# Kernel tuning notes

Hardware: AMD Instinct MI355X
Metric: run time of the kernel (lower is better)

## Reference

```python
import jax, jax.numpy as jnp
import numpy as np
import math

PHI = (1 + math.sqrt(5)) / 2
PI = math.pi
B, N, T, D, H = 2, 16, 512, 512, 8
DH = D // H
HALF = DH // 2
FF = int(D * PHI)  # 828
DC = D
PR_EPS = 1e-8
LN_EPS = 1e-5


def _ln(x, g, b):
    # x: (B,N,T,D); g,b: (N,D)
    mu = x.mean(axis=-1, keepdims=True)
    var = ((x - mu) ** 2).mean(axis=-1, keepdims=True)
    return (x - mu) * jax.lax.rsqrt(var + LN_EPS) * g[None, :, None, :] + b[None, :, None, :]


def _phase_resonance(a, b):
    # a, b: (B, N, D) in fp32; adjacent feature pairs = (re, im)
    pairs = a.shape[-1] // 2
    def to_phase(x):
        x2 = x.reshape(*x.shape[:-1], pairs, 2)
        return jnp.arctan2(x2[..., 1] + PR_EPS, x2[..., 0] + PR_EPS)
    ta, tb = to_phase(a), to_phase(b)
    delta = ta[..., :, None, :] - tb[..., None, :, :]  # (B, N, N, pairs)
    return jnp.cos(delta).mean(axis=-1)                # (B, N, N) in [-1, 1]


def setup_inputs():
    key = jax.random.key(0)
    ks = iter(jax.random.split(key, 24))
    w = lambda shape: jax.random.normal(next(ks), shape, jnp.float32) * 0.02
    return {
        'x': jax.random.normal(next(ks), (B, N, T, D), jnp.float32),
        'gate_w': w((N, D)),
        'gate_b': jnp.full((N,), 2.0, jnp.float32),  # torch init: bias=2.0
        'ln1_g': jnp.ones((N, D), jnp.float32),
        'ln1_b': jnp.zeros((N, D), jnp.float32),
        'wq': w((N, D, D)), 'wk': w((N, D, D)), 'wv': w((N, D, D)), 'wo': w((N, D, D)),
        'phase_angles': jnp.tile(jnp.linspace(0.0, PI, H, dtype=jnp.float32), (N, 1)),
        'ln2_g': jnp.ones((N, D), jnp.float32),
        'ln2_b': jnp.zeros((N, D), jnp.float32),
        'up_w': w((N, D, FF)), 'up_b': jnp.zeros((N, FF), jnp.float32),
        'down_w': w((N, FF, D)), 'down_b': jnp.zeros((N, D), jnp.float32),
        'commit_w': w((N, D)), 'commit_b': jnp.zeros((N,), jnp.float32),
        'center_w': w((N, D, DC)), 'center_b': jnp.zeros((N, DC), jnp.float32),
        'field_in_w': w((D, D)),
        'field_out_w': w((D, D)),
        'conductance': jnp.float32(1.0),
    }


def reference(x, gate_w, gate_b, ln1_g, ln1_b, wq, wk, wv, wo, phase_angles,
              ln2_g, ln2_b, up_w, up_b, down_w, down_b, commit_w, commit_b,
              center_w, center_b, field_in_w, field_out_w, conductance):
    # ---- BinaryAperture (straight-through binary gate) ----
    logits = jnp.einsum('bntd,nd->bnt', x, gate_w) + gate_b[None, :, None]
    prob = jax.nn.sigmoid(logits)  # temperature = 1.0
    hard = (prob > 0.5).astype(x.dtype)
    gate = (hard + prob - jax.lax.stop_gradient(prob))[..., None]  # (B,N,T,1)

    # ---- Field: phase-rotated, gated attention (scores forced to fp32) ----
    h = _ln(x, ln1_g, ln1_b)
    def proj(wm):
        z = jnp.einsum('bntd,nde->bnte', h, wm)
        return z.reshape(B, N, T, H, DH).transpose(0, 1, 3, 2, 4)  # (B,N,H,T,DH)
    Q, K, V = proj(wq), proj(wk), proj(wv)
    cos_a = jnp.cos(phase_angles)[None, :, :, None, None]  # (1,N,H,1,1)
    sin_a = jnp.sin(phase_angles)[None, :, :, None, None]
    def rot(Z):
        re, im = Z[..., :HALF], Z[..., HALF:2 * HALF]
        return jnp.concatenate([re * cos_a - im * sin_a, re * sin_a + im * cos_a], axis=-1)
    Q, K = rot(Q), rot(K)
    ge = gate[:, :, None]  # (B,N,1,T,1) broadcast over heads
    Q = Q * ge
    K = K * ge
    scores = jnp.einsum('bnhtd,bnhsd->bnhts', Q.astype(jnp.float32), K.astype(jnp.float32)) / math.sqrt(DH)
    attn = jax.nn.softmax(scores, axis=-1).astype(V.dtype)
    field = jnp.einsum('bnhts,bnhsd->bnhtd', attn, V)
    field = field.transpose(0, 1, 3, 2, 4).reshape(B, N, T, D)
    field = jnp.einsum('bntd,nde->bnte', field, wo) * gate
    x = x + field

    # ---- Boundary: golden-ratio FFN gated by commit * gate ----
    h2 = _ln(x, ln2_g, ln2_b)
    up = jax.nn.gelu(jnp.einsum('bntd,ndf->bntf', h2, up_w) + up_b[None, :, None], approximate=False)
    ff = jnp.einsum('bntf,nfd->bntd', up, down_w) + down_b[None, :, None]
    center_pool = x.mean(axis=2)  # (B,N,D) (pooled pre-FFN, as in torch)
    commit = jax.nn.sigmoid(jnp.einsum('bnd,nd->bn', center_pool, commit_w) + commit_b[None])  # (B,N)
    x = x + commit[..., None, None] * gate * ff
    center = jnp.tanh(jnp.einsum('bnd,nde->bne', center_pool, center_w) + center_b[None])  # (B,N,DC)

    # ---- SharedField: phase-resonance coupling across the N nodes ----
    node_gates = commit[..., None]  # (B,N,1)
    transmitted = center * node_gates
    h_res = jnp.einsum('bnd,de->bne', center, field_in_w).astype(jnp.float32)
    r_acc = _phase_resonance(h_res, h_res)  # (B,N,N); r_acc None -> r_acc_new = r_instant
    h_tx = jnp.einsum('bnd,de->bne', transmitted, field_in_w)
    recv = conductance * jnp.einsum('bmn,bnd->bmd', r_acc.astype(x.dtype), h_tx)
    field_signal = jnp.einsum('bnd,de->bne', recv, field_out_w)  # (B,N,D)

    # each node's boundary receives the field signal
    return x + field_signal[:, :, None, :]
```

## Files before the change

### kernel.cpp

```cpp
#include <hip/hip_runtime.h>

typedef unsigned short u16;
typedef __attribute__((ext_vector_type(8))) short short8;
typedef __attribute__((ext_vector_type(4))) float f32x4;

#define B_ 2
#define N_ 16
#define T_ 512
#define D_ 512
#define H_ 8
#define DH_ 64
#define HALF_ 32
#define FF_ 828
#define FFP_ 832
#define DC_ 512
#define LN_EPS 1e-5f
#define PR_EPS 1e-8f
#define NEG_INF (-3.0e38f)

__device__ __forceinline__ float b2f(u16 u) { return __uint_as_float(((unsigned)u) << 16); }
__device__ __forceinline__ u16 f2b(float f) {
  unsigned x = __float_as_uint(f);
  return (u16)((x + 0x7fffu + ((x >> 16) & 1u)) >> 16);
}
__device__ __forceinline__ float gelu_exact(float z) {
  return 0.5f * z * (1.f + erff(z * 0.70710678118654752f));
}

typedef __attribute__((address_space(1))) const unsigned GASu;
typedef __attribute__((address_space(3))) unsigned LASu;
__device__ __forceinline__ void gload_lds16(const void* g, void* l) {
  __builtin_amdgcn_global_load_lds((GASu*)g, (LASu*)l, 16, 0, 0);
}

__global__ __launch_bounds__(256) void ln_gate_kernel(
    const float* __restrict__ xsrc,
    const float* __restrict__ gate_w, const float* __restrict__ gate_b,
    const float* __restrict__ lng, const float* __restrict__ lnb,
    float* __restrict__ gate_out, u16* __restrict__ h_out, int do_gate) {
  __shared__ float red[256];
  int bnt = blockIdx.x;
  int n = (bnt / T_) % N_;
  int tid = threadIdx.x;
  const float* xr = xsrc + (size_t)bnt * D_;
  float x0 = xr[tid], x1 = xr[tid + 256];
  red[tid] = x0 + x1; __syncthreads();
  for (int s = 128; s > 0; s >>= 1) { if (tid < s) red[tid] += red[tid + s]; __syncthreads(); }
  float mu = red[0] * (1.f / D_); __syncthreads();
  float d0 = x0 - mu, d1 = x1 - mu;
  red[tid] = d0 * d0 + d1 * d1; __syncthreads();
  for (int s = 128; s > 0; s >>= 1) { if (tid < s) red[tid] += red[tid + s]; __syncthreads(); }
  float rstd = rsqrtf(red[0] * (1.f / D_) + LN_EPS); __syncthreads();
  if (do_gate) {
    red[tid] = x0 * gate_w[n * D_ + tid] + x1 * gate_w[n * D_ + tid + 256];
    __syncthreads();
    for (int s = 128; s > 0; s >>= 1) { if (tid < s) red[tid] += red[tid + s]; __syncthreads(); }
    if (tid == 0) gate_out[bnt] = (red[0] + gate_b[n] > 0.f) ? 1.f : 0.f;
  }
  size_t o = (size_t)bnt * D_;
  h_out[o + tid]       = f2b(d0 * rstd * lng[n * D_ + tid]       + lnb[n * D_ + tid]);
  h_out[o + tid + 256] = f2b(d1 * rstd * lng[n * D_ + tid + 256] + lnb[n * D_ + tid + 256]);
}

__global__ __launch_bounds__(256) void wconv_kernel(
    const float* __restrict__ W, u16* __restrict__ Wt, int Kd, int E, int Kpad) {
  __shared__ u16 tile[32][33];
  int e0 = blockIdx.x * 32, k0 = blockIdx.y * 32, n = blockIdx.z;
  const float* Wb = W + (size_t)n * Kd * E;
  u16* Wtb = Wt + (size_t)n * E * Kpad;
  int r = threadIdx.x >> 3, c4 = (threadIdx.x & 7) * 4;
  int kk = k0 + r;
  if (kk < Kd) {
    if (e0 + c4 + 3 < E) {
      float4 w4 = *(const float4*)(Wb + (size_t)kk * E + e0 + c4);
      tile[r][c4 + 0] = f2b(w4.x); tile[r][c4 + 1] = f2b(w4.y);
      tile[r][c4 + 2] = f2b(w4.z); tile[r][c4 + 3] = f2b(w4.w);
    } else {
      #pragma unroll
      for (int j = 0; j < 4; ++j) {
        int ee = e0 + c4 + j;
        tile[r][c4 + j] = (ee < E) ? f2b(Wb[(size_t)kk * E + ee]) : (u16)0;
      }
    }
  } else {
    #pragma unroll
    for (int j = 0; j < 4; ++j) tile[r][c4 + j] = 0;
  }
  __syncthreads();
  int ee = e0 + r;
  if (ee < E) {
    u16* dst = Wtb + (size_t)ee * Kpad + k0 + c4;
    if (k0 + c4 + 3 < Kpad) {
      ushort4 o;
      o.x = tile[c4 + 0][r]; o.y = tile[c4 + 1][r];
      o.z = tile[c4 + 2][r]; o.w = tile[c4 + 3][r];
      *(ushort4*)dst = o;
    } else {
      #pragma unroll
      for (int j = 0; j < 4; ++j) if (k0 + c4 + j < Kpad) dst[j] = tile[c4 + j][r];
    }
  }
}

#define BM 128
#define BN 128
#define BK 32
__global__ __launch_bounds__(256) void gemm_mfma_kernel(
    const u16* __restrict__ In,
    const float* __restrict__ W0, const float* __restrict__ W1, const float* __restrict__ W2,
    const u16* __restrict__ Wt0, const u16* __restrict__ Wt1, const u16* __restrict__ Wt2,
    u16* __restrict__ O0, u16* __restrict__ O1, u16* __restrict__ O2,
    float* __restrict__ OutF,
    int Kd, int KdW, int E, int Es, int mode,
    const float* __restrict__ bias,
    const float* __restrict__ xres, const float* __restrict__ gate) {
  __shared__ __align__(16) u16 As[BM * BK];
  __shared__ __align__(16) u16 Bs[BN * BK];
  int z = blockIdx.z;
  int bn = z & 31, proj = z >> 5;
  int n = bn & (N_ - 1);
  const float* W = (proj == 0) ? W0 : ((proj == 1) ? W1 : W2);
  const u16* Wt = (proj == 0) ? Wt0 : ((proj == 1) ? Wt1 : Wt2);
  u16* Out = (proj == 0) ? O0 : ((proj == 1) ? O1 : O2);
  int e0 = blockIdx.x * BN, t0 = blockIdx.y * BM;
  int tid = threadIdx.x;
  int lane = tid & 63, wave = tid >> 6;
  int m_off = (wave & 1) * 64, n_off = (wave >> 1) * 64;
  int ml = lane & 15, quad = lane >> 4;
  const u16* Inb = In + (size_t)bn * T_ * Kd;
  const float* Wb = W ? W + (size_t)n * (size_t)KdW * E : nullptr;
  const u16* Wtb = Wt ? Wt + (size_t)n * E * Kd : nullptr;

  int srow = (wave * 2) * 16 + (lane >> 2);
  int sg0 = (lane & 3) ^ ((srow >> 1) & 3);
  int sg1 = (lane & 3) ^ (((srow + 16) >> 1) & 3);
  int swz = (quad ^ ((ml >> 1) & 3)) * 8;

  f32x4 acc[4][4] = {};

  int ksteps = (Kd + BK - 1) / BK;
  for (int ks = 0; ks < ksteps; ++ks) {
    int k0 = ks * BK;
    if (Wtb) {
      int i0 = wave * 2;
      gload_lds16(Inb + (size_t)(t0 + srow) * Kd + k0 + sg0 * 8, &As[i0 * 512]);
      gload_lds16(Inb + (size_t)(t0 + srow + 16) * Kd + k0 + sg1 * 8, &As[(i0 + 1) * 512]);
      gload_lds16(Wtb + (size_t)(e0 + srow) * Kd + k0 + sg0 * 8, &Bs[i0 * 512]);
      gload_lds16(Wtb + (size_t)(e0 + srow + 16) * Kd + k0 + sg1 * 8, &Bs[(i0 + 1) * 512]);
    } else {
      #pragma unroll
      for (int it = 0; it < 2; ++it) {
        int slot = tid * 2 + it;
        int r = slot >> 2;
        int q = slot & 3;
        int kg = k0 + q * 8;
        const u16* src = Inb + (size_t)(t0 + r) * Kd + kg;
        u16* dst = &As[r * BK + (q ^ ((r >> 1) & 3)) * 8];
        if (kg + 8 <= Kd) {
          *(short8*)dst = *(const short8*)src;
        } else {
          #pragma unroll
          for (int xx = 0; xx < 8; ++xx) dst[xx] = (kg + xx < Kd) ? src[xx] : (u16)0;
        }
      }
      {
        int kk = tid & 31;
        int eb = (tid >> 5) * 16;
        int kg = k0 + kk;
        int s = kk >> 3, w = kk & 7;
        #pragma unroll
        for (int it = 0; it < 4; ++it) {
          int e = eb + it * 4;
          int eg = e0 + e;
          float4 w4 = {0.f, 0.f, 0.f, 0.f};
          if (kg < KdW && eg < E) w4 = *(const float4*)(Wb + (size_t)kg * E + eg);
          Bs[(e + 0) * BK + ((s ^ (((e + 0) >> 1) & 3)) * 8) + w] = f2b(w4.x);
          Bs[(e + 1) * BK + ((s ^ (((e + 1) >> 1) & 3)) * 8) + w] = f2b(w4.y);
          Bs[(e + 2) * BK + ((s ^ (((e + 2) >> 1) & 3)) * 8) + w] = f2b(w4.z);
          Bs[(e + 3) * BK + ((s ^ (((e + 3) >> 1) & 3)) * 8) + w] = f2b(w4.w);
        }
      }
    }
    __syncthreads();
    short8 a[4], b[4];
    #pragma unroll
    for (int i = 0; i < 4; ++i)
      a[i] = *(const short8*)&As[(m_off + i * 16 + ml) * BK + swz];
    #pragma unroll
    for (int j = 0; j < 4; ++j)
      b[j] = *(const short8*)&Bs[(n_off + j * 16 + ml) * BK + swz];
    #pragma unroll
    for (int i = 0; i < 4; ++i)
      #pragma unroll
      for (int j = 0; j < 4; ++j)
        acc[i][j] = __builtin_amdgcn_mfma_f32_16x16x32_bf16(a[i], b[j], acc[i][j], 0, 0, 0);
    __syncthreads();
  }

  #pragma unroll
  for (int j = 0; j < 4; ++j) {
    int eg = e0 + n_off + j * 16 + ml;
    if (eg >= Es) continue;
    #pragma unroll
    for (int i = 0; i < 4; ++i) {
      #pragma unroll
      for (int r = 0; r < 4; ++r) {
        int tg = t0 + m_off + i * 16 + quad * 4 + r;
        float v = acc[i][j][r];
        size_t o = (size_t)bn * T_ * Es + (size_t)tg * Es + eg;
        if (mode == 0) {
          Out[o] = f2b(v);
        } else if (mode == 1) {
          float g = gate[(size_t)bn * T_ + tg];
          OutF[o] = xres[o] + v * g;
        } else if (mode == 2) {
          Out[o] = (eg < E) ? f2b(gelu_exact(v + bias[(size_t)n * E + eg])) : (u16)0;
        } else {
          Out[o] = f2b(v + bias[(size_t)n * E + eg]);
        }
      }
    }
  }
}

__global__ __launch_bounds__(256) void rot_gate_kernel(
    u16* __restrict__ q, u16* __restrict__ k,
    const float* __restrict__ phase, const float* __restrict__ gate) {
  long long i = (long long)blockIdx.x * 256 + threadIdx.x;
  int c = (int)(i & 31);
  int h = (int)((i >> 5) & 7);
  int t = (int)((i >> 8) & 511);
  int bn = (int)(i >> 17);
  int n = bn & (N_ - 1);
  float a = phase[n * H_ + h];
  float ca = cosf(a), sa = sinf(a);
  float g = gate[(size_t)bn * T_ + t];
  size_t base = ((size_t)bn * T_ + t) * D_ + h * DH_;
  float qr = b2f(q[base + c]), qi = b2f(q[base + c + HALF_]);
  q[base + c]         = f2b((qr * ca - qi * sa) * g);
  q[base + c + HALF_] = f2b((qr * sa + qi * ca) * g);
  float kr = b2f(k[base + c]), ki = b2f(k[base + c + HALF_]);
  k[base + c]         = f2b((kr * ca - ki * sa) * g);
  k[base + c + HALF_] = f2b((kr * sa + ki * ca) * g);
}

#define ATS 72
__global__ __launch_bounds__(256) void attn_kernel(
    const u16* __restrict__ Q, const u16* __restrict__ K, const u16* __restrict__ V,
    u16* __restrict__ O) {
  __shared__ __align__(16) u16 Qs[64 * ATS];
  __shared__ __align__(16) u16 Ks[64 * ATS];
  __shared__ __align__(16) u16 Vs[64 * ATS];
  __shared__ __align__(16) u16 Ps[64 * ATS];
  int qt = blockIdx.x, h = blockIdx.y, bn = blockIdx.z;
  int tid = threadIdx.x;
  int lane = tid & 63, wave = tid >> 6;
  int ml = lane & 15, quad = lane >> 4;
  int t0 = qt * 64;
  size_t rowbase = (size_t)bn * T_ * D_ + (size_t)h * DH_;

  {
    int r = tid >> 2;
    int c = (tid & 3) * 16;
    const u16* src = Q + rowbase + (size_t)(t0 + r) * D_ + c;
    #pragma unroll
    for (int hf = 0; hf < 2; ++hf) {
      short8 v = *(const short8*)(src + hf * 8);
      #pragma unroll
      for (int e = 0; e < 8; ++e)
        ((u16*)&v)[e] = f2b(b2f(((u16*)&v)[e]) * 0.125f);
      *(short8*)&Qs[r * ATS + c + hf * 8] = v;
    }
  }

  float m_[4], l_[4];
  f32x4 acco[4] = {};
  #pragma unroll
  for (int r = 0; r < 4; ++r) { m_[r] = NEG_INF; l_[r] = 0.f; }

  for (int sc = 0; sc < 8; ++sc) {
    int s0 = sc * 64;
    {
      int r = tid >> 2;
      int c = (tid & 3) * 16;
      const u16* src = K + rowbase + (size_t)(s0 + r) * D_ + c;
      *(short8*)&Ks[r * ATS + c]     = *(const short8*)(src);
      *(short8*)&Ks[r * ATS + c + 8] = *(const short8*)(src + 8);
    }
    {
      int sw = wave * 16;
      const u16* src = V + rowbase + (size_t)(s0 + sw) * D_ + lane;
      short8 v0, v1;
      #pragma unroll
      for (int r = 0; r < 8; ++r) ((u16*)&v0)[r] = src[(size_t)r * D_];
      #pragma unroll
      for (int r = 0; r < 8; ++r) ((u16*)&v1)[r] = src[(size_t)(r + 8) * D_];
      *(short8*)&Vs[lane * ATS + sw]     = v0;
      *(short8*)&Vs[lane * ATS + sw + 8] = v1;
    }
    __syncthreads();

    f32x4 s4[4] = {};
    #pragma unroll
    for (int kst = 0; kst < 2; ++kst) {
      short8 a = *(const short8*)&Qs[(wave * 16 + ml) * ATS + kst * 32 + quad * 8];
      #pragma unroll
      for (int j = 0; j < 4; ++j) {
        short8 b = *(const short8*)&Ks[(j * 16 + ml) * ATS + kst * 32 + quad * 8];
        s4[j] = __builtin_amdgcn_mfma_f32_16x16x32_bf16(a, b, s4[j], 0, 0, 0);
      }
    }

    #pragma unroll
    for (int r = 0; r < 4; ++r) {
      float cm = fmaxf(fmaxf(s4[0][r], s4[1][r]), fmaxf(s4[2][r], s4[3][r]));
      #pragma unroll
      for (int off = 1; off < 16; off <<= 1) cm = fmaxf(cm, __shfl_xor(cm, off));
      float mn = fmaxf(m_[r], cm);
      float al = expf(m_[r] - mn);
      u16 q0 = f2b(expf(s4[0][r] - mn)), q1 = f2b(expf(s4[1][r] - mn));
      u16 q2 = f2b(expf(s4[2][r] - mn)), q3 = f2b(expf(s4[3][r] - mn));
      float rs = b2f(q0) + b2f(q1) + b2f(q2) + b2f(q3);
      #pragma unroll
      for (int off = 1; off < 16; off <<= 1) rs += __shfl_xor(rs, off);
      l_[r] = l_[r] * al + rs;
      m_[r] = mn;
      #pragma unroll
      for (int jd = 0; jd < 4; ++jd) acco[jd][r] *= al;
      int trow = wave * 16 + quad * 4 + r;
      Ps[trow * ATS + 0 * 16 + ml] = q0;
      Ps[trow * ATS + 1 * 16 + ml] = q1;
      Ps[trow * ATS + 2 * 16 + ml] = q2;
      Ps[trow * ATS + 3 * 16 + ml] = q3;
    }

    #pragma unroll
    for (int sst = 0; sst < 2; ++sst) {
      short8 a = *(const short8*)&Ps[(wave * 16 + ml) * ATS + sst * 32 + quad * 8];
      #pragma unroll
      for (int jd = 0; jd < 4; ++jd) {
        short8 b = *(const short8*)&Vs[(jd * 16 + ml) * ATS + sst * 32 + quad * 8];
        acco[jd] = __builtin_amdgcn_mfma_f32_16x16x32_bf16(a, b, acco[jd], 0, 0, 0);
      }
    }
    __syncthreads();
  }

  #pragma unroll
  for (int r = 0; r < 4; ++r) {
    float inv = 1.f / l_[r];
    int trow = t0 + wave * 16 + quad * 4 + r;
    #pragma unroll
    for (int jd = 0; jd < 4; ++jd)
      O[rowbase + (size_t)trow * D_ + jd * 16 + ml] = f2b(acco[jd][r] * inv);
  }
}

__global__ __launch_bounds__(256) void pool_kernel(const float* __restrict__ x2, float* __restrict__ cp) {
  int bid = blockIdx.x;
  int bn = bid >> 1;
  int d = (bid & 1) * 256 + threadIdx.x;
  const float* base = x2 + (size_t)bn * T_ * D_ + d;
  float s = 0.f;
  for (int t = 0; t < T_; ++t) s += base[(size_t)t * D_];
  cp[(size_t)bn * D_ + d] = s * (1.f / T_);
}

__global__ __launch_bounds__(256) void commit_center_kernel(
    const float* __restrict__ cp, const float* __restrict__ commit_w, const float* __restrict__ commit_b,
    const float* __restrict__ center_w, const float* __restrict__ center_b,
    float* __restrict__ commit, float* __restrict__ center) {
  __shared__ float cps[512];
  __shared__ float red[256];
  int bn = blockIdx.x, n = bn % N_, tid = threadIdx.x;
  cps[tid] = cp[(size_t)bn * D_ + tid];
  cps[tid + 256] = cp[(size_t)bn * D_ + tid + 256];
  __syncthreads();
  red[tid] = cps[tid] * commit_w[n * D_ + tid] + cps[tid + 256] * commit_w[n * D_ + tid + 256];
  __syncthreads();
  for (int s = 128; s > 0; s >>= 1) { if (tid < s) red[tid] += red[tid + s]; __syncthreads(); }
  if (tid == 0) commit[bn] = 1.f / (1.f + expf(-(red[0] + commit_b[n])));
  #pragma unroll
  for (int eo = 0; eo < 2; ++eo) {
    int e = eo * 256 + tid;
    float acc = center_b[(size_t)n * DC_ + e];
    for (int d = 0; d < D_; ++d) acc = fmaf(cps[d], center_w[((size_t)n * D_ + d) * DC_ + e], acc);
    center[(size_t)bn * DC_ + e] = tanhf(acc);
  }
}

__global__ __launch_bounds__(256) void matvec_kernel(
    const float* __restrict__ inp, const float* __restrict__ Wm, float* __restrict__ outp) {
  __shared__ float s[512];
  int bn = blockIdx.x, tid = threadIdx.x;
  s[tid] = inp[(size_t)bn * D_ + tid];
  s[tid + 256] = inp[(size_t)bn * D_ + tid + 256];
  __syncthreads();
  #pragma unroll
  for (int eo = 0; eo < 2; ++eo) {
    int e = eo * 256 + tid;
    float acc = 0.f;
    for (int d = 0; d < D_; ++d) acc = fmaf(s[d], Wm[(size_t)d * D_ + e], acc);
    outp[(size_t)bn * D_ + e] = acc;
  }
}

__global__ __launch_bounds__(256) void uv_kernel(
    const float* __restrict__ hres, float* __restrict__ u, float* __restrict__ v) {
  int i = blockIdx.x * 256 + threadIdx.x;
  float xr = hres[2 * i] + PR_EPS;
  float yi = hres[2 * i + 1] + PR_EPS;
  float r = sqrtf(xr * xr + yi * yi);
  u[i] = xr / r; v[i] = yi / r;
}

__global__ __launch_bounds__(256) void racc_kernel(
    const float* __restrict__ u, const float* __restrict__ v, float* __restrict__ ra) {
  int b = blockIdx.x, tid = threadIdx.x;
  int mm = tid >> 4, nn = tid & 15;
  const float* ub = u + (size_t)b * N_ * 256;
  const float* vb = v + (size_t)b * N_ * 256;
  float acc = 0.f;
  for (int p = 0; p < 256; ++p)
    acc += ub[mm * 256 + p] * ub[nn * 256 + p] + vb[mm * 256 + p] * vb[nn * 256 + p];
  ra[(size_t)b * N_ * N_ + mm * N_ + nn] = acc * (1.f / 256.f);
}

__global__ __launch_bounds__(256) void recv_kernel(
    const float* __restrict__ ra, const float* __restrict__ commit,
    const float* __restrict__ hres, const float* __restrict__ cond, float* __restrict__ recv) {
  int bn = blockIdx.x, b = bn / N_, mm = bn % N_, tid = threadIdx.x;
  float c = cond[0];
  #pragma unroll
  for (int eo = 0; eo < 2; ++eo) {
    int d = eo * 256 + tid;
    float acc = 0.f;
    for (int nn = 0; nn < N_; ++nn)
      acc += ra[(size_t)b * N_ * N_ + mm * N_ + nn] * commit[b * N_ + nn] *
             hres[((size_t)b * N_ + nn) * D_ + d];
    recv[(size_t)bn * D_ + d] = c * acc;
  }
}

__global__ __launch_bounds__(256) void final_kernel(
    const float* __restrict__ x2, const float* __restrict__ commit,
    const float* __restrict__ gate, const u16* __restrict__ ff,
    const float* __restrict__ fs, float* __restrict__ out) {
  long long i4 = (long long)blockIdx.x * 256 + threadIdx.x;
  long long base = i4 * 4;
  int d = (int)(base & (D_ - 1));
  int t = (int)((base >> 9) & (T_ - 1));
  int bn = (int)(base >> 18);
  float cg = commit[bn] * gate[(size_t)bn * T_ + t];
  float4 xv = *(const float4*)(x2 + base);
  ushort4 fv = *(const ushort4*)(ff + base);
  float4 sv = *(const float4*)(fs + (size_t)bn * D_ + d);
  float4 r;
  r.x = xv.x + cg * b2f(fv.x) + sv.x;
  r.y = xv.y + cg * b2f(fv.y) + sv.y;
  r.z = xv.z + cg * b2f(fv.z) + sv.z;
  r.w = xv.w + cg * b2f(fv.w) + sv.w;
  *(float4*)(out + base) = r;
}

extern "C" void kernel_launch(void* const* d_in, const int* in_sizes, int n_in,
                              void* d_out, int out_size, void* d_ws, size_t ws_size,
                              hipStream_t stream) {
  (void)in_sizes; (void)n_in; (void)out_size;
  const float* x          = (const float*)d_in[0];
  const float* gate_w     = (const float*)d_in[1];
  const float* gate_b     = (const float*)d_in[2];
  const float* ln1_g      = (const float*)d_in[3];
  const float* ln1_b      = (const float*)d_in[4];
  const float* wq         = (const float*)d_in[5];
  const float* wk         = (const float*)d_in[6];
  const float* wv         = (const float*)d_in[7];
  const float* wo         = (const float*)d_in[8];
  const float* phase      = (const float*)d_in[9];
  const float* ln2_g      = (const float*)d_in[10];
  const float* ln2_b      = (const float*)d_in[11];
  const float* up_w       = (const float*)d_in[12];
  const float* up_b       = (const float*)d_in[13];
  const float* down_w     = (const float*)d_in[14];
  const float* down_b     = (const float*)d_in[15];
  const float* commit_w   = (const float*)d_in[16];
  const float* commit_b   = (const float*)d_in[17];
  const float* center_w   = (const float*)d_in[18];
  const float* center_b   = (const float*)d_in[19];
  const float* field_in_w = (const float*)d_in[20];
  const float* field_out_w= (const float*)d_in[21];
  const float* cond       = (const float*)d_in[22];

  const long long BNTD = 8388608LL;
  u16* w16 = (u16*)d_ws;
  u16* R0 = w16;
  u16* R1 = w16 + BNTD;
  u16* R2 = w16 + 2 * BNTD;
  u16* R3 = w16 + 3 * BNTD;
  float* sm   = (float*)(w16 + 4 * BNTD);
  float* gate   = sm;
  float* cp     = sm + 16384;
  float* center = sm + 2 * 16384;
  float* hres   = sm + 3 * 16384;
  float* uu     = sm + 4 * 16384;
  float* vv     = uu + 8192;
  float* ra     = vv + 8192;
  float* recvb  = ra + 512;
  float* fsig   = recvb + 16384;
  float* commit = fsig + 16384;
  float* x2 = (float*)d_out;

  const size_t WSQ = (size_t)N_ * 512 * 512;
  const size_t WUPu = (size_t)N_ * 828 * 512;
  const size_t WUPd = (size_t)N_ * 512 * 832;
  u16* wtbase = (u16*)(sm + 115232);
  u16* wtq = wtbase;
  u16* wtk = wtq + WSQ;
  u16* wtv = wtk + WSQ;
  u16* wto = wtv + WSQ;
  u16* wtu = wto + WSQ;
  u16* wtd = wtu + WUPu;
  size_t needed = (size_t)((char*)(wtd + WUPd) - (char*)d_ws);
  bool use_wt = ws_size >= needed;

  ln_gate_kernel<<<16384, 256, 0, stream>>>(x, gate_w, gate_b, ln1_g, ln1_b, gate, R0, 1);

  if (use_wt) {
    wconv_kernel<<<dim3(16, 16, 16), 256, 0, stream>>>(wq, wtq, 512, 512, 512);
    wconv_kernel<<<dim3(16, 16, 16), 256, 0, stream>>>(wk, wtk, 512, 512, 512);
    wconv_kernel<<<dim3(16, 16, 16), 256, 0, stream>>>(wv, wtv, 512, 512, 512);
    wconv_kernel<<<dim3(16, 16, 16), 256, 0, stream>>>(wo, wto, 512, 512, 512);
    wconv_kernel<<<dim3(26, 16, 16), 256, 0, stream>>>(up_w, wtu, 512, 828, 512);
    wconv_kernel<<<dim3(16, 26, 16), 256, 0, stream>>>(down_w, wtd, 828, 512, 832);
  }
  const u16* pq = use_wt ? wtq : nullptr;
  const u16* pk = use_wt ? wtk : nullptr;
  const u16* pv = use_wt ? wtv : nullptr;
  const u16* po = use_wt ? wto : nullptr;
  const u16* pu = use_wt ? wtu : nullptr;
  const u16* pd = use_wt ? wtd : nullptr;

  gemm_mfma_kernel<<<dim3(4, 4, 96), 256, 0, stream>>>(
      R0, wq, wk, wv, pq, pk, pv, R1, R2, R3, nullptr,
      512, 512, 512, 512, 0, nullptr, nullptr, nullptr);
  rot_gate_kernel<<<16384, 256, 0, stream>>>(R1, R2, phase, gate);
  attn_kernel<<<dim3(8, 8, 32), 256, 0, stream>>>(R1, R2, R3, R0);
  gemm_mfma_kernel<<<dim3(4, 4, 32), 256, 0, stream>>>(
      R0, wo, nullptr, nullptr, po, nullptr, nullptr, nullptr, nullptr, nullptr, x2,
      512, 512, 512, 512, 1, nullptr, x, gate);
  ln_gate_kernel<<<16384, 256, 0, stream>>>(x2, nullptr, nullptr, ln2_g, ln2_b, nullptr, R1, 0);
  gemm_mfma_kernel<<<dim3(7, 4, 32), 256, 0, stream>>>(
      R1, up_w, nullptr, nullptr, pu, nullptr, nullptr, R2, nullptr, nullptr, nullptr,
      512, 512, 828, 832, 2, up_b, nullptr, nullptr);
  gemm_mfma_kernel<<<dim3(4, 4, 32), 256, 0, stream>>>(
      R2, down_w, nullptr, nullptr, pd, nullptr, nullptr, R0, nullptr, nullptr, nullptr,
      832, 828, 512, 512, 3, down_b, nullptr, nullptr);
  pool_kernel<<<64, 256, 0, stream>>>(x2, cp);
  commit_center_kernel<<<32, 256, 0, stream>>>(cp, commit_w, commit_b, center_w, center_b, commit, center);
  matvec_kernel<<<32, 256, 0, stream>>>(center, field_in_w, hres);
  uv_kernel<<<32, 256, 0, stream>>>(hres, uu, vv);
  racc_kernel<<<2, 256, 0, stream>>>(uu, vv, ra);
  recv_kernel<<<32, 256, 0, stream>>>(ra, commit, hres, cond, recvb);
  matvec_kernel<<<32, 256, 0, stream>>>(recvb, field_out_w, fsig);
  final_kernel<<<8192, 256, 0, stream>>>(x2, commit, gate, R0, fsig, x2);
}
```

Baseline: 812.0 us.

## Use wave-shuffle LayerNorm, pre-transposed V, lazy softmax rescale, split pooling

LayerNorm and gate reductions move from shared-memory tree loops to wave shuffles with fewer barriers. A new transpose kernel writes V as (bh, dh, T) so attention loads it with vector loads instead of strided scalar loads. The query scaling by 0.125 moves into the rotary kernel, and the online softmax rescales only when the running max grows, using fast exp. Mean pooling becomes a two-stage parallel reduction with far more blocks. The costs are an extra V transpose pass and extra workspace, and the fast exp may change numerics slightly.

```diff
diff --git a/kernel.cpp b/kernel.cpp
--- a/kernel.cpp
+++ b/kernel.cpp
@@ -38,25 +38,34 @@
     const float* __restrict__ gate_w, const float* __restrict__ gate_b,
     const float* __restrict__ lng, const float* __restrict__ lnb,
     float* __restrict__ gate_out, u16* __restrict__ h_out, int do_gate) {
-  __shared__ float red[256];
+  __shared__ float redA[4], redB[4], redC[4];
   int bnt = blockIdx.x;
   int n = (bnt / T_) % N_;
   int tid = threadIdx.x;
+  int lane = tid & 63, wave = tid >> 6;
   const float* xr = xsrc + (size_t)bnt * D_;
   float x0 = xr[tid], x1 = xr[tid + 256];
-  red[tid] = x0 + x1; __syncthreads();
-  for (int s = 128; s > 0; s >>= 1) { if (tid < s) red[tid] += red[tid + s]; __syncthreads(); }
-  float mu = red[0] * (1.f / D_); __syncthreads();
+  float s = x0 + x1;
+  #pragma unroll
+  for (int off = 32; off > 0; off >>= 1) s += __shfl_xor(s, off);
+  if (lane == 0) redA[wave] = s;
+  if (do_gate) {
+    float t = x0 * gate_w[n * D_ + tid] + x1 * gate_w[n * D_ + tid + 256];
+    #pragma unroll
+    for (int off = 32; off > 0; off >>= 1) t += __shfl_xor(t, off);
+    if (lane == 0) redC[wave] = t;
+  }
+  __syncthreads();
+  float mu = (redA[0] + redA[1] + redA[2] + redA[3]) * (1.f / D_);
   float d0 = x0 - mu, d1 = x1 - mu;
-  red[tid] = d0 * d0 + d1 * d1; __syncthreads();
-  for (int s = 128; s > 0; s >>= 1) { if (tid < s) red[tid] += red[tid + s]; __syncthreads(); }
-  float rstd = rsqrtf(red[0] * (1.f / D_) + LN_EPS); __syncthreads();
-  if (do_gate) {
-    red[tid] = x0 * gate_w[n * D_ + tid] + x1 * gate_w[n * D_ + tid + 256];
-    __syncthreads();
-    for (int s = 128; s > 0; s >>= 1) { if (tid < s) red[tid] += red[tid + s]; __syncthreads(); }
-    if (tid == 0) gate_out[bnt] = (red[0] + gate_b[n] > 0.f) ? 1.f : 0.f;
-  }
+  float v = d0 * d0 + d1 * d1;
+  #pragma unroll
+  for (int off = 32; off > 0; off >>= 1) v += __shfl_xor(v, off);
+  if (lane == 0) redB[wave] = v;
+  __syncthreads();
+  float rstd = rsqrtf((redB[0] + redB[1] + redB[2] + redB[3]) * (1.f / D_) + LN_EPS);
+  if (do_gate && tid == 0)
+    gate_out[bnt] = (redC[0] + redC[1] + redC[2] + redC[3] + gate_b[n] > 0.f) ? 1.f : 0.f;
   size_t o = (size_t)bnt * D_;
   h_out[o + tid]       = f2b(d0 * rstd * lng[n * D_ + tid]       + lnb[n * D_ + tid]);
   h_out[o + tid + 256] = f2b(d1 * rstd * lng[n * D_ + tid + 256] + lnb[n * D_ + tid + 256]);
@@ -100,6 +109,23 @@
       for (int j = 0; j < 4; ++j) if (k0 + c4 + j < Kpad) dst[j] = tile[c4 + j][r];
     }
   }
+}
+
+__global__ __launch_bounds__(256) void vtrans_kernel(const u16* __restrict__ V, u16* __restrict__ Vt) {
+  __shared__ u16 tile[32][36];
+  int tt0 = blockIdx.x * 32;
+  int dd0 = blockIdx.y * 32;
+  int bh = blockIdx.z;
+  int bn = bh >> 3, h = bh & 7;
+  const u16* src = V + (size_t)bn * T_ * D_ + h * DH_;
+  int r = threadIdx.x >> 3, c4 = (threadIdx.x & 7) * 4;
+  *(ushort4*)&tile[r][c4] = *(const ushort4*)(src + (size_t)(tt0 + r) * D_ + dd0 + c4);
+  __syncthreads();
+  u16* dst = Vt + ((size_t)bh * DH_ + dd0 + r) * T_ + tt0 + c4;
+  ushort4 o;
+  o.x = tile[c4 + 0][r]; o.y = tile[c4 + 1][r];
+  o.z = tile[c4 + 2][r]; o.w = tile[c4 + 3][r];
+  *(ushort4*)dst = o;
 }
 
 #define BM 128
@@ -237,8 +263,10 @@
   float g = gate[(size_t)bn * T_ + t];
   size_t base = ((size_t)bn * T_ + t) * D_ + h * DH_;
   float qr = b2f(q[base + c]), qi = b2f(q[base + c + HALF_]);
-  q[base + c]         = f2b((qr * ca - qi * sa) * g);
-  q[base + c + HALF_] = f2b((qr * sa + qi * ca) * g);
+  u16 a0 = f2b((qr * ca - qi * sa) * g);
+  u16 a1 = f2b((qr * sa + qi * ca) * g);
+  q[base + c]         = f2b(b2f(a0) * 0.125f);
+  q[base + c + HALF_] = f2b(b2f(a1) * 0.125f);
   float kr = b2f(k[base + c]), ki = b2f(k[base + c + HALF_]);
   k[base + c]         = f2b((kr * ca - ki * sa) * g);
   k[base + c + HALF_] = f2b((kr * sa + ki * ca) * g);
@@ -247,7 +275,7 @@
 #define ATS 72
 __global__ __launch_bounds__(256) void attn_kernel(
     const u16* __restrict__ Q, const u16* __restrict__ K, const u16* __restrict__ V,
-    u16* __restrict__ O) {
+    const u16* __restrict__ Vt, u16* __restrict__ O) {
   __shared__ __align__(16) u16 Qs[64 * ATS];
   __shared__ __align__(16) u16 Ks[64 * ATS];
   __shared__ __align__(16) u16 Vs[64 * ATS];
@@ -258,43 +286,41 @@
   int ml = lane & 15, quad = lane >> 4;
   int t0 = qt * 64;
   size_t rowbase = (size_t)bn * T_ * D_ + (size_t)h * DH_;
+  int r = tid >> 2;
+  int c = (tid & 3) * 16;
 
   {
-    int r = tid >> 2;
-    int c = (tid & 3) * 16;
     const u16* src = Q + rowbase + (size_t)(t0 + r) * D_ + c;
-    #pragma unroll
-    for (int hf = 0; hf < 2; ++hf) {
-      short8 v = *(const short8*)(src + hf * 8);
-      #pragma unroll
-      for (int e = 0; e < 8; ++e)
-        ((u16*)&v)[e] = f2b(b2f(((u16*)&v)[e]) * 0.125f);
-      *(short8*)&Qs[r * ATS + c + hf * 8] = v;
-    }
-  }
+    *(short8*)&Qs[r * ATS + c]     = *(const short8*)(src);
+    *(short8*)&Qs[r * ATS + c + 8] = *(const short8*)(src + 8);
+  }
+  const u16* ksrc = K + rowbase + (size_t)r * D_ + c;
+  const u16* vsrc = Vt ? (Vt + ((size_t)(bn * H_ + h) * DH_ + r) * T_ + c) : nullptr;
 
   float m_[4], l_[4];
   f32x4 acco[4] = {};
   #pragma unroll
-  for (int r = 0; r < 4; ++r) { m_[r] = NEG_INF; l_[r] = 0.f; }
+  for (int rr = 0; rr < 4; ++rr) { m_[rr] = NEG_INF; l_[rr] = 0.f; }
 
   for (int sc = 0; sc < 8; ++sc) {
     int s0 = sc * 64;
     {
-      int r = tid >> 2;
-      int c = (tid & 3) * 16;
-      const u16* src = K + rowbase + (size_t)(s0 + r) * D_ + c;
-      *(short8*)&Ks[r * ATS + c]     = *(const short8*)(src);
-      *(short8*)&Ks[r * ATS + c + 8] = *(const short8*)(src + 8);
-    }
-    {
+      const u16* kp = ksrc + (size_t)s0 * D_;
+      *(short8*)&Ks[r * ATS + c]     = *(const short8*)(kp);
+      *(short8*)&Ks[r * ATS + c + 8] = *(const short8*)(kp + 8);
+    }
+    if (Vt) {
+      const u16* vp = vsrc + s0;
+      *(short8*)&Vs[r * ATS + c]     = *(const short8*)(vp);
+      *(short8*)&Vs[r * ATS + c + 8] = *(const short8*)(vp + 8);
+    } else {
       int sw = wave * 16;
       const u16* src = V + rowbase + (size_t)(s0 + sw) * D_ + lane;
       short8 v0, v1;
       #pragma unroll
-      for (int r = 0; r < 8; ++r) ((u16*)&v0)[r] = src[(size_t)r * D_];
-      #pragma unroll
-      for (int r = 0; r < 8; ++r) ((u16*)&v1)[r] = src[(size_t)(r + 8) * D_];
+      for (int rr = 0; rr < 8; ++rr) ((u16*)&v0)[rr] = src[(size_t)rr * D_];
+      #pragma unroll
+      for (int rr = 0; rr < 8; ++rr) ((u16*)&v1)[rr] = src[(size_t)(rr + 8) * D_];
       *(short8*)&Vs[lane * ATS + sw]     = v0;
       *(short8*)&Vs[lane * ATS + sw + 8] = v1;
     }
@@ -312,22 +338,24 @@
     }
 
     #pragma unroll
-    for (int r = 0; r < 4; ++r) {
-      float cm = fmaxf(fmaxf(s4[0][r], s4[1][r]), fmaxf(s4[2][r], s4[3][r]));
+    for (int rr = 0; rr < 4; ++rr) {
+      float cm = fmaxf(fmaxf(s4[0][rr], s4[1][rr]), fmaxf(s4[2][rr], s4[3][rr]));
       #pragma unroll
       for (int off = 1; off < 16; off <<= 1) cm = fmaxf(cm, __shfl_xor(cm, off));
-      float mn = fmaxf(m_[r], cm);
-      float al = expf(m_[r] - mn);
-      u16 q0 = f2b(expf(s4[0][r] - mn)), q1 = f2b(expf(s4[1][r] - mn));
-      u16 q2 = f2b(expf(s4[2][r] - mn)), q3 = f2b(expf(s4[3][r] - mn));
+      if (cm > m_[rr]) {
+        float al = __expf(m_[rr] - cm);
+        l_[rr] *= al;
+        #pragma unroll
+        for (int jd = 0; jd < 4; ++jd) acco[jd][rr] *= al;
+        m_[rr] = cm;
+      }
+      u16 q0 = f2b(__expf(s4[0][rr] - m_[rr])), q1 = f2b(__expf(s4[1][rr] - m_[rr]));
+      u16 q2 = f2b(__expf(s4[2][rr] - m_[rr])), q3 = f2b(__expf(s4[3][rr] - m_[rr]));
       float rs = b2f(q0) + b2f(q1) + b2f(q2) + b2f(q3);
       #pragma unroll
       for (int off = 1; off < 16; off <<= 1) rs += __shfl_xor(rs, off);
-      l_[r] = l_[r] * al + rs;
-      m_[r] = mn;
-      #pragma unroll
-      for (int jd = 0; jd < 4; ++jd) acco[jd][r] *= al;
-      int trow = wave * 16 + quad * 4 + r;
+      l_[rr] += rs;
+      int trow = wave * 16 + quad * 4 + rr;
       Ps[trow * ATS + 0 * 16 + ml] = q0;
       Ps[trow * ATS + 1 * 16 + ml] = q1;
       Ps[trow * ATS + 2 * 16 + ml] = q2;
@@ -347,23 +375,37 @@
   }
 
   #pragma unroll
-  for (int r = 0; r < 4; ++r) {
-    float inv = 1.f / l_[r];
-    int trow = t0 + wave * 16 + quad * 4 + r;
+  for (int rr = 0; rr < 4; ++rr) {
+    float inv = 1.f / l_[rr];
+    int trow = t0 + wave * 16 + quad * 4 + rr;
     #pragma unroll
     for (int jd = 0; jd < 4; ++jd)
-      O[rowbase + (size_t)trow * D_ + jd * 16 + ml] = f2b(acco[jd][r] * inv);
-  }
-}
-
-__global__ __launch_bounds__(256) void pool_kernel(const float* __restrict__ x2, float* __restrict__ cp) {
-  int bid = blockIdx.x;
-  int bn = bid >> 1;
-  int d = (bid & 1) * 256 + threadIdx.x;
-  const float* base = x2 + (size_t)bn * T_ * D_ + d;
-  float s = 0.f;
-  for (int t = 0; t < T_; ++t) s += base[(size_t)t * D_];
-  cp[(size_t)bn * D_ + d] = s * (1.f / T_);
+      O[rowbase + (size_t)trow * D_ + jd * 16 + ml] = f2b(acco[jd][rr] * inv);
+  }
+}
+
+__global__ __launch_bounds__(256) void pool1_kernel(const float* __restrict__ x2, float* __restrict__ part) {
+  int tc = blockIdx.x & 15, bn = blockIdx.x >> 4;
+  int d = threadIdx.x;
+  const float* base = x2 + ((size_t)bn * T_ + tc * 32) * D_;
+  float s0 = 0.f, s1 = 0.f;
+  for (int t = 0; t < 32; ++t) {
+    s0 += base[(size_t)t * D_ + d];
+    s1 += base[(size_t)t * D_ + d + 256];
+  }
+  float* p = part + ((size_t)bn * 16 + tc) * D_;
+  p[d] = s0; p[d + 256] = s1;
+}
+__global__ __launch_bounds__(256) void pool2_kernel(const float* __restrict__ part, float* __restrict__ cp) {
+  int bn = blockIdx.x;
+  int d = threadIdx.x;
+  float s0 = 0.f, s1 = 0.f;
+  for (int tc = 0; tc < 16; ++tc) {
+    s0 += part[((size_t)bn * 16 + tc) * D_ + d];
+    s1 += part[((size_t)bn * 16 + tc) * D_ + d + 256];
+  }
+  cp[(size_t)bn * D_ + d]       = s0 * (1.f / T_);
+  cp[(size_t)bn * D_ + d + 256] = s1 * (1.f / T_);
 }
 
 __global__ __launch_bounds__(256) void commit_center_kernel(
@@ -508,19 +550,21 @@
   float* recvb  = ra + 512;
   float* fsig   = recvb + 16384;
   float* commit = fsig + 16384;
+  float* part   = sm + 115232;
   float* x2 = (float*)d_out;
 
   const size_t WSQ = (size_t)N_ * 512 * 512;
   const size_t WUPu = (size_t)N_ * 828 * 512;
   const size_t WUPd = (size_t)N_ * 512 * 832;
-  u16* wtbase = (u16*)(sm + 115232);
+  u16* wtbase = (u16*)(sm + 115232 + 262144);
   u16* wtq = wtbase;
   u16* wtk = wtq + WSQ;
   u16* wtv = wtk + WSQ;
   u16* wto = wtv + WSQ;
   u16* wtu = wto + WSQ;
   u16* wtd = wtu + WUPu;
-  size_t needed = (size_t)((char*)(wtd + WUPd) - (char*)d_ws);
+  u16* vtb = wtd + WUPd;
+  size_t needed = (size_t)((char*)(vtb + BNTD) - (char*)d_ws);
   bool use_wt = ws_size >= needed;
 
   ln_gate_kernel<<<16384, 256, 0, stream>>>(x, gate_w, gate_b, ln1_g, ln1_b, gate, R0, 1);
@@ -544,7 +588,8 @@
       R0, wq, wk, wv, pq, pk, pv, R1, R2, R3, nullptr,
       512, 512, 512, 512, 0, nullptr, nullptr, nullptr);
   rot_gate_kernel<<<16384, 256, 0, stream>>>(R1, R2, phase, gate);
-  attn_kernel<<<dim3(8, 8, 32), 256, 0, stream>>>(R1, R2, R3, R0);
+  if (use_wt) vtrans_kernel<<<dim3(16, 2, 256), 256, 0, stream>>>(R3, vtb);
+  attn_kernel<<<dim3(8, 8, 32), 256, 0, stream>>>(R1, R2, R3, use_wt ? vtb : nullptr, R0);
   gemm_mfma_kernel<<<dim3(4, 4, 32), 256, 0, stream>>>(
       R0, wo, nullptr, nullptr, po, nullptr, nullptr, nullptr, nullptr, nullptr, x2,
       512, 512, 512, 512, 1, nullptr, x, gate);
@@ -555,7 +600,8 @@
   gemm_mfma_kernel<<<dim3(4, 4, 32), 256, 0, stream>>>(
       R2, down_w, nullptr, nullptr, pd, nullptr, nullptr, R0, nullptr, nullptr, nullptr,
       832, 828, 512, 512, 3, down_b, nullptr, nullptr);
-  pool_kernel<<<64, 256, 0, stream>>>(x2, cp);
+  pool1_kernel<<<512, 256, 0, stream>>>(x2, part);
+  pool2_kernel<<<32, 256, 0, stream>>>(part, cp);
   commit_center_kernel<<<32, 256, 0, stream>>>(cp, commit_w, commit_b, center_w, center_b, commit, center);
   matvec_kernel<<<32, 256, 0, stream>>>(center, field_in_w, hres);
   uv_kernel<<<32, 256, 0, stream>>>(hres, uu, vv);
```

New measurement: 786.2 us. 1.03x faster.
